# Performance work log

Measured on AMD Instinct MI355X. Metric: run time of the kernel, lower is better.

## Reference

```python
import jax, jax.numpy as jnp
import numpy as np

V, E, H, O, S, N = 32000, 256, 512, 32000, 128, 256

def setup_inputs() -> dict:
    key = jax.random.key(0)
    ks = jax.random.split(key, 12)
    s = 0.05
    return {
        'x': jax.random.randint(ks[0], (N, 1), 0, V),
        'encoder_outputs': jax.random.normal(ks[1], (N, S, 2 * H), jnp.float32),
        'hidden': jax.random.normal(ks[2], (1, N, H), jnp.float32),
        'cell': jax.random.normal(ks[3], (1, N, H), jnp.float32),
        'emb': jax.random.normal(ks[4], (V, E), jnp.float32) * s,
        'W_energy': jax.random.normal(ks[5], (1, 3 * H), jnp.float32) * s,
        'b_energy': jnp.zeros((1,), jnp.float32),
        'W_ih': jax.random.normal(ks[6], (4 * H, E + 2 * H), jnp.float32) * s,
        'W_hh': jax.random.normal(ks[7], (4 * H, H), jnp.float32) * s,
        'b_ih': jnp.zeros((4 * H,), jnp.float32),
        'b_hh': jnp.zeros((4 * H,), jnp.float32),
        'W_out': jax.random.normal(ks[8], (O, H), jnp.float32) * s,
        'b_out': jnp.zeros((O,), jnp.float32),
    }

def reference(x, encoder_outputs, hidden, cell, emb, W_energy, b_energy,
              W_ih, W_hh, b_ih, b_hh, W_out, b_out):
    # Dropout is identity at inference (eval mode).
    embedding = emb[x]                      # [N,1,E]
    n, s, _ = encoder_outputs.shape
    h = hidden[0]                            # [N,H] (num_layers==1)
    h_rep = jnp.broadcast_to(h[:, None, :], (n, s, h.shape[-1]))  # [N,S,H]
    feat = jnp.concatenate([h_rep, encoder_outputs], axis=-1)     # [N,S,3H]
    energy = jax.nn.relu(feat @ W_energy.T + b_energy)            # [N,S,1]
    attention = jax.nn.softmax(energy, axis=1)                    # softmax over seq
    context = jnp.einsum('nsk,nsl->nkl', attention, encoder_outputs)  # [N,1,2H]
    lstm_in = jnp.concatenate([context, embedding], axis=-1)[:, 0, :]  # [N,E+2H]
    gates = lstm_in @ W_ih.T + b_ih + h @ W_hh.T + b_hh           # [N,4H]
    i, f, g, o = jnp.split(gates, 4, axis=-1)                     # torch gate order
    i, f, o = jax.nn.sigmoid(i), jax.nn.sigmoid(f), jax.nn.sigmoid(o)
    g = jnp.tanh(g)
    c_new = f * cell[0] + i * g
    h_new = o * jnp.tanh(c_new)
    outputs = h_new[:, None, :]                                   # [N,1,H]
    predictions = outputs @ W_out.T + b_out                       # [N,1,O]
    return predictions, h_new[None], c_new[None]
```

## Files before the change

kernel.cpp:

```cpp
#include <hip/hip_runtime.h>
#include <hip/hip_bf16.h>

#define N_ 256
#define S_ 128
#define H_ 512
#define E_ 256
#define O_ 32000
#define KZ 1792
#define GJ 2048
#define KSPLIT 4
#define KCHUNK 448

typedef __attribute__((ext_vector_type(8))) short sv8;
typedef __attribute__((ext_vector_type(4))) float fv4;

__device__ __forceinline__ unsigned short f2bf(float f) {
  return __builtin_bit_cast(unsigned short, __float2bfloat16(f));
}

__device__ __forceinline__ sv8 pack8(fv4 a, fv4 b) {
  sv8 r;
  r[0] = (short)f2bf(a[0]); r[1] = (short)f2bf(a[1]);
  r[2] = (short)f2bf(a[2]); r[3] = (short)f2bf(a[3]);
  r[4] = (short)f2bf(b[0]); r[5] = (short)f2bf(b[1]);
  r[6] = (short)f2bf(b[2]); r[7] = (short)f2bf(b[3]);
  return r;
}

__global__ __launch_bounds__(1024) void k_attn(
    const int* __restrict__ x, const float* __restrict__ eo,
    const float* __restrict__ hid, const float* __restrict__ emb,
    const float* __restrict__ We, const float* __restrict__ be,
    const float* __restrict__ Wih, const float* __restrict__ Whh,
    unsigned short* __restrict__ Wgbf, unsigned short* __restrict__ z)
{
  if (blockIdx.y == 1) {
    const int tid = blockIdx.x * 1024 + threadIdx.x;
    for (int g = tid; g < 2048 * 224; g += 256 * 1024) {
      const int j = g / 224, c = g - j * 224;
      sv8* dst = (sv8*)(Wgbf + (size_t)j * KZ);
      if (c < 160) {
        const fv4* src = (const fv4*)(Wih + (size_t)j * 1280);
        dst[c] = pack8(src[2 * c], src[2 * c + 1]);
      } else {
        const int cc = c - 160;
        const fv4* src = (const fv4*)(Whh + (size_t)j * 512);
        dst[c] = pack8(src[2 * cc], src[2 * cc + 1]);
      }
    }
    return;
  }

  const int n = blockIdx.x;
  const int t = threadIdx.x;
  const int w = t >> 6;
  const int l = t & 63;

  __shared__ float s_red[16];
  __shared__ float s_l[16];
  __shared__ float s_ctx[16][1024];

  float hv = (t < 512) ? hid[(size_t)n * H_ + t] * We[t] : 0.f;
  #pragma unroll
  for (int off = 32; off >= 1; off >>= 1) hv += __shfl_xor(hv, off);
  if (l == 0) s_red[w] = hv;
  __syncthreads();
  float hWe = be[0];
  #pragma unroll
  for (int i = 0; i < 8; ++i) hWe += s_red[i];

  fv4 we0, we1, we2, we3;
  {
    const fv4* wp = (const fv4*)(We + H_);
    we0 = wp[l]; we1 = wp[l + 64]; we2 = wp[l + 128]; we3 = wp[l + 192];
  }

  float lsum = 0.f;
  fv4 c0 = {0,0,0,0}, c1 = {0,0,0,0}, c2 = {0,0,0,0}, c3 = {0,0,0,0};
  const float* eob = eo + ((size_t)n * S_ + w * 8) * 1024;
  #pragma unroll 2
  for (int i = 0; i < 8; ++i) {
    const fv4* p = (const fv4*)(eob + (size_t)i * 1024);
    fv4 v0 = p[l], v1 = p[l + 64], v2 = p[l + 128], v3 = p[l + 192];
    float d = 0.f;
    #pragma unroll
    for (int c = 0; c < 4; ++c)
      d += v0[c]*we0[c] + v1[c]*we1[c] + v2[c]*we2[c] + v3[c]*we3[c];
    #pragma unroll
    for (int off = 32; off >= 1; off >>= 1) d += __shfl_xor(d, off);
    const float pp = __expf(fmaxf(d + hWe, 0.f));
    lsum += pp;
    #pragma unroll
    for (int c = 0; c < 4; ++c) {
      c0[c] += pp*v0[c];
      c1[c] += pp*v1[c];
      c2[c] += pp*v2[c];
      c3[c] += pp*v3[c];
    }
  }
  if (l == 0) s_l[w] = lsum;
  {
    fv4* sc_ = (fv4*)s_ctx[w];
    sc_[l] = c0; sc_[l+64] = c1; sc_[l+128] = c2; sc_[l+192] = c3;
  }
  __syncthreads();

  float L = 0.f;
  #pragma unroll
  for (int i = 0; i < 16; ++i) L += s_l[i];
  const float rL = 1.f / L;

  float acc = 0.f;
  #pragma unroll
  for (int i = 0; i < 16; ++i) acc += s_ctx[i][t];
  unsigned short* zr = z + (size_t)n * KZ;
  zr[t] = f2bf(acc * rL);

  if (t < 256)       zr[1024 + t] = f2bf(emb[(size_t)x[n] * E_ + t]);
  else if (t < 768)  zr[1024 + t] = f2bf(hid[(size_t)n * H_ + (t - 256)]);
}

__global__ __launch_bounds__(256) void k_gates(
    const unsigned short* __restrict__ z, const unsigned short* __restrict__ Wgbf,
    float* __restrict__ part)
{
  const int j0 = blockIdx.x * 64;
  const int n0 = blockIdx.y * 64;
  const int kc = blockIdx.z * KCHUNK;
  const int t = threadIdx.x;
  const int w = t >> 6, l = t & 63;
  const int lr = l & 15, lg = l >> 4;
  const int jb = j0 + w * 16 + lr;

  const unsigned short* arow = z + kc + 8 * lg;
  const unsigned short* wrow = Wgbf + (size_t)jb * KZ + kc + 8 * lg;

  fv4 acc[4] = {{0,0,0,0},{0,0,0,0},{0,0,0,0},{0,0,0,0}};
  #pragma unroll
  for (int s = 0; s < 14; ++s) {
    const sv8 bf = *(const sv8*)(wrow + s * 32);
    #pragma unroll
    for (int f = 0; f < 4; ++f) {
      const sv8 af = *(const sv8*)(arow + (size_t)(n0 + f*16 + lr) * KZ + s * 32);
      acc[f] = __builtin_amdgcn_mfma_f32_16x16x32_bf16(af, bf, acc[f], 0, 0, 0);
    }
  }
  float* pp = part + (size_t)blockIdx.z * (N_ * GJ);
  #pragma unroll
  for (int f = 0; f < 4; ++f) {
    #pragma unroll
    for (int r = 0; r < 4; ++r)
      pp[(size_t)(n0 + f*16 + lg*4 + r) * GJ + jb] = acc[f][r];
  }
}

__global__ __launch_bounds__(256) void k_lstm(
    const float* __restrict__ part, const float* __restrict__ cell,
    const float* __restrict__ bih, const float* __restrict__ bhh,
    float* __restrict__ hout, float* __restrict__ cout,
    unsigned short* __restrict__ hbf)
{
  const int tid = blockIdx.x * 256 + threadIdx.x;
  const int n = tid >> 9, hh = tid & 511;
  const size_t base = (size_t)n * GJ;
  float ig = bih[hh]        + bhh[hh];
  float fg = bih[512 + hh]  + bhh[512 + hh];
  float gg = bih[1024 + hh] + bhh[1024 + hh];
  float og = bih[1536 + hh] + bhh[1536 + hh];
  #pragma unroll
  for (int k = 0; k < KSPLIT; ++k) {
    const float* p = part + (size_t)k * (N_ * GJ) + base;
    ig += p[hh];
    fg += p[512 + hh];
    gg += p[1024 + hh];
    og += p[1536 + hh];
  }
  ig = 1.f / (1.f + __expf(-ig));
  fg = 1.f / (1.f + __expf(-fg));
  og = 1.f / (1.f + __expf(-og));
  gg = tanhf(gg);
  const float c = fg * cell[tid] + ig * gg;
  const float h = og * tanhf(c);
  cout[tid] = c;
  hout[tid] = h;
  hbf[tid] = f2bf(h);
}

__global__ __launch_bounds__(512, 2) void k_pred(
    const unsigned short* __restrict__ hbf, const float* __restrict__ Wout,
    const float* __restrict__ bout, float* __restrict__ pred)
{
  __shared__ unsigned short Blds[64 * 512];
  const int o0 = blockIdx.x * 64;
  const int t = threadIdx.x;

  #pragma unroll
  for (int i = 0; i < 8; ++i) {
    const int g = t + i * 512;
    const int row = g >> 6, c = g & 63;
    const fv4* src = (const fv4*)(Wout + (size_t)(o0 + row) * H_ + c * 8);
    const sv8 v = pack8(src[0], src[1]);
    *(sv8*)((char*)Blds + row * 1024 + ((c * 16) ^ ((row & 7) << 4))) = v;
  }
  __syncthreads();

  const int w = t >> 6, l = t & 63;
  const int lr = l & 15, lg = l >> 4;
  const int nr = w * 32;

  fv4 acc[2][4] = {};
  #pragma unroll
  for (int kk = 0; kk < 16; ++kk) {
    sv8 a[2];
    #pragma unroll
    for (int f = 0; f < 2; ++f)
      a[f] = *(const sv8*)(hbf + (size_t)(nr + f*16 + lr) * H_ + kk*32 + 8*lg);
    #pragma unroll
    for (int fo = 0; fo < 4; ++fo) {
      const int row = fo * 16 + lr;
      const sv8 b = *(const sv8*)((const char*)Blds + row * 1024 +
                                  ((kk*64 + lg*16) ^ ((row & 7) << 4)));
      #pragma unroll
      for (int f = 0; f < 2; ++f)
        acc[f][fo] = __builtin_amdgcn_mfma_f32_16x16x32_bf16(a[f], b, acc[f][fo], 0, 0, 0);
    }
  }
  #pragma unroll
  for (int fo = 0; fo < 4; ++fo) {
    const int oo = o0 + fo*16 + lr;
    const float bo = bout[oo];
    #pragma unroll
    for (int f = 0; f < 2; ++f) {
      #pragma unroll
      for (int r = 0; r < 4; ++r)
        pred[(size_t)(nr + f*16 + lg*4 + r) * O_ + oo] = acc[f][fo][r] + bo;
    }
  }
}

extern "C" void kernel_launch(void* const* d_in, const int* in_sizes, int n_in,
                              void* d_out, int out_size, void* d_ws, size_t ws_size,
                              hipStream_t stream) {
  const int*   x    = (const int*)  d_in[0];
  const float* eo   = (const float*)d_in[1];
  const float* hid  = (const float*)d_in[2];
  const float* cell = (const float*)d_in[3];
  const float* emb  = (const float*)d_in[4];
  const float* We   = (const float*)d_in[5];
  const float* be   = (const float*)d_in[6];
  const float* Wih  = (const float*)d_in[7];
  const float* Whh  = (const float*)d_in[8];
  const float* bih  = (const float*)d_in[9];
  const float* bhh  = (const float*)d_in[10];
  const float* Wout = (const float*)d_in[11];
  const float* bout = (const float*)d_in[12];

  float* pred = (float*)d_out;
  float* hout = pred + (size_t)N_ * O_;
  float* cout = hout + (size_t)N_ * H_;

  unsigned short* z    = (unsigned short*)d_ws;
  unsigned short* hbf  = z + (size_t)N_ * KZ;
  float* part = (float*)(hbf + (size_t)N_ * H_);
  unsigned short* Wgbf = (unsigned short*)(part + (size_t)KSPLIT * N_ * GJ);

  k_attn <<<dim3(256, 2), 1024, 0, stream>>>(x, eo, hid, emb, We, be,
                                             Wih, Whh, Wgbf, z);
  k_gates<<<dim3(32, 4, KSPLIT), 256, 0, stream>>>(z, Wgbf, part);
  k_lstm <<<512, 256, 0, stream>>>(part, cell, bih, bhh, hout, cout, hbf);
  k_pred <<<500, 512, 0, stream>>>(hbf, Wout, bout, pred);
}
```

Before: 89.35 us.

## Fuse attention, gates, LSTM and projection into one cooperative persistent kernel

```diff
diff --git a/kernel.cpp b/kernel.cpp
--- a/kernel.cpp
+++ b/kernel.cpp
@@ -1,5 +1,8 @@
 #include <hip/hip_runtime.h>
 #include <hip/hip_bf16.h>
+#include <hip/hip_cooperative_groups.h>
+
+namespace cg = cooperative_groups;
 
 #define N_ 256
 #define S_ 128
@@ -8,8 +11,8 @@
 #define O_ 32000
 #define KZ 1792
 #define GJ 2048
-#define KSPLIT 4
-#define KCHUNK 448
+#define KSPLIT 8
+#define KCHUNK 224
 
 typedef __attribute__((ext_vector_type(8))) short sv8;
 typedef __attribute__((ext_vector_type(4))) float fv4;
@@ -27,16 +30,126 @@
   return r;
 }
 
-__global__ __launch_bounds__(1024) void k_attn(
+__device__ __forceinline__ void pred_stage(const float* __restrict__ Wout, int o0,
+                                           unsigned char* buf, int t) {
+  #pragma unroll
+  for (int i = 0; i < 4; ++i) {
+    const int g = t + i * 1024;
+    const int row = g >> 6, c = g & 63;
+    const fv4* src = (const fv4*)(Wout + (size_t)(o0 + row) * H_ + c * 8);
+    const sv8 v = pack8(src[0], src[1]);
+    *(sv8*)(buf + row * 1024 + ((c * 16) ^ ((row & 7) << 4))) = v;
+  }
+}
+
+__device__ __forceinline__ void pred_compute(const unsigned short* __restrict__ hbf,
+    const float* __restrict__ bout, float* __restrict__ pred, int o0,
+    const unsigned char* buf, int w, int lr, int lg) {
+  const int nr = w * 16;
+  fv4 acc[4] = {};
+  #pragma unroll
+  for (int kk = 0; kk < 16; ++kk) {
+    const sv8 a = *(const sv8*)(hbf + (size_t)(nr + lr) * H_ + kk * 32 + 8 * lg);
+    #pragma unroll
+    for (int fo = 0; fo < 4; ++fo) {
+      const int row = fo * 16 + lr;
+      const sv8 bb = *(const sv8*)(buf + row * 1024 +
+                                   ((kk * 64 + lg * 16) ^ ((row & 7) << 4)));
+      acc[fo] = __builtin_amdgcn_mfma_f32_16x16x32_bf16(a, bb, acc[fo], 0, 0, 0);
+    }
+  }
+  #pragma unroll
+  for (int fo = 0; fo < 4; ++fo) {
+    const int oo = o0 + fo * 16 + lr;
+    const float bo = bout[oo];
+    #pragma unroll
+    for (int r = 0; r < 4; ++r)
+      pred[(size_t)(nr + lg * 4 + r) * O_ + oo] = acc[fo][r] + bo;
+  }
+}
+
+__global__ __launch_bounds__(1024) void k_mega(
     const int* __restrict__ x, const float* __restrict__ eo,
-    const float* __restrict__ hid, const float* __restrict__ emb,
-    const float* __restrict__ We, const float* __restrict__ be,
-    const float* __restrict__ Wih, const float* __restrict__ Whh,
-    unsigned short* __restrict__ Wgbf, unsigned short* __restrict__ z)
+    const float* __restrict__ hid, const float* __restrict__ cell,
+    const float* __restrict__ emb, const float* __restrict__ We,
+    const float* __restrict__ be, const float* __restrict__ Wih,
+    const float* __restrict__ Whh, const float* __restrict__ bih,
+    const float* __restrict__ bhh, const float* __restrict__ Wout,
+    const float* __restrict__ bout,
+    unsigned short* __restrict__ z, unsigned short* __restrict__ hbf,
+    float* __restrict__ part, unsigned short* __restrict__ Wgbf,
+    float* __restrict__ pred, float* __restrict__ hout, float* __restrict__ cout)
 {
-  if (blockIdx.y == 1) {
-    const int tid = blockIdx.x * 1024 + threadIdx.x;
-    for (int g = tid; g < 2048 * 224; g += 256 * 1024) {
+  cg::grid_group grid = cg::this_grid();
+  const int b = blockIdx.x;
+  const int t = threadIdx.x;
+  const int w = t >> 6, l = t & 63;
+  const int lr = l & 15, lg = l >> 4;
+
+  __shared__ __align__(16) unsigned char smem[131072];
+  __shared__ float s_red[16], s_l[16];
+
+  {
+    const int n = b;
+    float* s_ctx = (float*)smem;
+
+    float hv = (t < 512) ? hid[(size_t)n * H_ + t] * We[t] : 0.f;
+    #pragma unroll
+    for (int off = 32; off >= 1; off >>= 1) hv += __shfl_xor(hv, off);
+    if (l == 0) s_red[w] = hv;
+    __syncthreads();
+    float hWe = be[0];
+    #pragma unroll
+    for (int i = 0; i < 8; ++i) hWe += s_red[i];
+
+    fv4 we0, we1, we2, we3;
+    {
+      const fv4* wp = (const fv4*)(We + H_);
+      we0 = wp[l]; we1 = wp[l + 64]; we2 = wp[l + 128]; we3 = wp[l + 192];
+    }
+
+    float lsum = 0.f;
+    fv4 c0 = {0,0,0,0}, c1 = {0,0,0,0}, c2 = {0,0,0,0}, c3 = {0,0,0,0};
+    const float* eob = eo + ((size_t)n * S_ + w * 8) * 1024;
+    #pragma unroll 2
+    for (int i = 0; i < 8; ++i) {
+      const fv4* p = (const fv4*)(eob + (size_t)i * 1024);
+      fv4 v0 = p[l], v1 = p[l + 64], v2 = p[l + 128], v3 = p[l + 192];
+      float d = 0.f;
+      #pragma unroll
+      for (int c = 0; c < 4; ++c)
+        d += v0[c]*we0[c] + v1[c]*we1[c] + v2[c]*we2[c] + v3[c]*we3[c];
+      #pragma unroll
+      for (int off = 32; off >= 1; off >>= 1) d += __shfl_xor(d, off);
+      const float pp = __expf(fmaxf(d + hWe, 0.f));
+      lsum += pp;
+      #pragma unroll
+      for (int c = 0; c < 4; ++c) {
+        c0[c] += pp*v0[c]; c1[c] += pp*v1[c];
+        c2[c] += pp*v2[c]; c3[c] += pp*v3[c];
+      }
+    }
+    if (l == 0) s_l[w] = lsum;
+    {
+      fv4* sc_ = (fv4*)(s_ctx + w * 1024);
+      sc_[l] = c0; sc_[l+64] = c1; sc_[l+128] = c2; sc_[l+192] = c3;
+    }
+    __syncthreads();
+
+    float L = 0.f;
+    #pragma unroll
+    for (int i = 0; i < 16; ++i) L += s_l[i];
+    const float rL = 1.f / L;
+
+    float acc = 0.f;
+    #pragma unroll
+    for (int i = 0; i < 16; ++i) acc += s_ctx[i * 1024 + t];
+    unsigned short* zr = z + (size_t)n * KZ;
+    zr[t] = f2bf(acc * rL);
+    if (t < 256)       zr[1024 + t] = f2bf(emb[(size_t)x[n] * E_ + t]);
+    else if (t < 768)  zr[1024 + t] = f2bf(hid[(size_t)n * H_ + (t - 256)]);
+
+    for (int g = b * 1024 + t; g < 2048 * 224; g += 256 * 1024) {
       const int j = g / 224, c = g - j * 224;
       sv8* dst = (sv8*)(Wgbf + (size_t)j * KZ);
       if (c < 160) {
@@ -48,192 +161,82 @@
         dst[c] = pack8(src[2 * cc], src[2 * cc + 1]);
       }
     }
-    return;
-  }
-
-  const int n = blockIdx.x;
-  const int t = threadIdx.x;
-  const int w = t >> 6;
-  const int l = t & 63;
-
-  __shared__ float s_red[16];
-  __shared__ float s_l[16];
-  __shared__ float s_ctx[16][1024];
-
-  float hv = (t < 512) ? hid[(size_t)n * H_ + t] * We[t] : 0.f;
-  #pragma unroll
-  for (int off = 32; off >= 1; off >>= 1) hv += __shfl_xor(hv, off);
-  if (l == 0) s_red[w] = hv;
-  __syncthreads();
-  float hWe = be[0];
-  #pragma unroll
-  for (int i = 0; i < 8; ++i) hWe += s_red[i];
-
-  fv4 we0, we1, we2, we3;
-  {
-    const fv4* wp = (const fv4*)(We + H_);
-    we0 = wp[l]; we1 = wp[l + 64]; we2 = wp[l + 128]; we3 = wp[l + 192];
-  }
-
-  float lsum = 0.f;
-  fv4 c0 = {0,0,0,0}, c1 = {0,0,0,0}, c2 = {0,0,0,0}, c3 = {0,0,0,0};
-  const float* eob = eo + ((size_t)n * S_ + w * 8) * 1024;
-  #pragma unroll 2
-  for (int i = 0; i < 8; ++i) {
-    const fv4* p = (const fv4*)(eob + (size_t)i * 1024);
-    fv4 v0 = p[l], v1 = p[l + 64], v2 = p[l + 128], v3 = p[l + 192];
-    float d = 0.f;
-    #pragma unroll
-    for (int c = 0; c < 4; ++c)
-      d += v0[c]*we0[c] + v1[c]*we1[c] + v2[c]*we2[c] + v3[c]*we3[c];
-    #pragma unroll
-    for (int off = 32; off >= 1; off >>= 1) d += __shfl_xor(d, off);
-    const float pp = __expf(fmaxf(d + hWe, 0.f));
-    lsum += pp;
-    #pragma unroll
-    for (int c = 0; c < 4; ++c) {
-      c0[c] += pp*v0[c];
-      c1[c] += pp*v1[c];
-      c2[c] += pp*v2[c];
-      c3[c] += pp*v3[c];
-    }
-  }
-  if (l == 0) s_l[w] = lsum;
-  {
-    fv4* sc_ = (fv4*)s_ctx[w];
-    sc_[l] = c0; sc_[l+64] = c1; sc_[l+128] = c2; sc_[l+192] = c3;
-  }
-  __syncthreads();
-
-  float L = 0.f;
-  #pragma unroll
-  for (int i = 0; i < 16; ++i) L += s_l[i];
-  const float rL = 1.f / L;
-
-  float acc = 0.f;
-  #pragma unroll
-  for (int i = 0; i < 16; ++i) acc += s_ctx[i][t];
-  unsigned short* zr = z + (size_t)n * KZ;
-  zr[t] = f2bf(acc * rL);
-
-  if (t < 256)       zr[1024 + t] = f2bf(emb[(size_t)x[n] * E_ + t]);
-  else if (t < 768)  zr[1024 + t] = f2bf(hid[(size_t)n * H_ + (t - 256)]);
-}
-
-__global__ __launch_bounds__(256) void k_gates(
-    const unsigned short* __restrict__ z, const unsigned short* __restrict__ Wgbf,
-    float* __restrict__ part)
-{
-  const int j0 = blockIdx.x * 64;
-  const int n0 = blockIdx.y * 64;
-  const int kc = blockIdx.z * KCHUNK;
-  const int t = threadIdx.x;
-  const int w = t >> 6, l = t & 63;
-  const int lr = l & 15, lg = l >> 4;
-  const int jb = j0 + w * 16 + lr;
-
-  const unsigned short* arow = z + kc + 8 * lg;
-  const unsigned short* wrow = Wgbf + (size_t)jb * KZ + kc + 8 * lg;
-
-  fv4 acc[4] = {{0,0,0,0},{0,0,0,0},{0,0,0,0},{0,0,0,0}};
-  #pragma unroll
-  for (int s = 0; s < 14; ++s) {
-    const sv8 bf = *(const sv8*)(wrow + s * 32);
+  }
+  grid.sync();
+
+  {
+    const int quad = w >> 2, wq = w & 3;
+    const int tile = b * 4 + quad;
+    const int j0   = (tile & 31) * 64;
+    const int rest = tile >> 5;
+    const int n0   = (rest & 3) * 64;
+    const int kidx = rest >> 2;
+    const int kc   = kidx * KCHUNK;
+    const int jb   = j0 + wq * 16 + lr;
+
+    const unsigned short* arow = z + kc + 8 * lg;
+    const unsigned short* wrow = Wgbf + (size_t)jb * KZ + kc + 8 * lg;
+
+    fv4 acc[4] = {{0,0,0,0},{0,0,0,0},{0,0,0,0},{0,0,0,0}};
+    #pragma unroll
+    for (int s = 0; s < 7; ++s) {
+      const sv8 bf = *(const sv8*)(wrow + s * 32);
+      #pragma unroll
+      for (int f = 0; f < 4; ++f) {
+        const sv8 af = *(const sv8*)(arow + (size_t)(n0 + f*16 + lr) * KZ + s * 32);
+        acc[f] = __builtin_amdgcn_mfma_f32_16x16x32_bf16(af, bf, acc[f], 0, 0, 0);
+      }
+    }
+    float* pp = part + (size_t)kidx * (N_ * GJ);
     #pragma unroll
     for (int f = 0; f < 4; ++f) {
-      const sv8 af = *(const sv8*)(arow + (size_t)(n0 + f*16 + lr) * KZ + s * 32);
-      acc[f] = __builtin_amdgcn_mfma_f32_16x16x32_bf16(af, bf, acc[f], 0, 0, 0);
-    }
-  }
-  float* pp = part + (size_t)blockIdx.z * (N_ * GJ);
-  #pragma unroll
-  for (int f = 0; f < 4; ++f) {
-    #pragma unroll
-    for (int r = 0; r < 4; ++r)
-      pp[(size_t)(n0 + f*16 + lg*4 + r) * GJ + jb] = acc[f][r];
-  }
-}
-
-__global__ __launch_bounds__(256) void k_lstm(
-    const float* __restrict__ part, const float* __restrict__ cell,
-    const float* __restrict__ bih, const float* __restrict__ bhh,
-    float* __restrict__ hout, float* __restrict__ cout,
-    unsigned short* __restrict__ hbf)
-{
-  const int tid = blockIdx.x * 256 + threadIdx.x;
-  const int n = tid >> 9, hh = tid & 511;
-  const size_t base = (size_t)n * GJ;
-  float ig = bih[hh]        + bhh[hh];
-  float fg = bih[512 + hh]  + bhh[512 + hh];
-  float gg = bih[1024 + hh] + bhh[1024 + hh];
-  float og = bih[1536 + hh] + bhh[1536 + hh];
-  #pragma unroll
-  for (int k = 0; k < KSPLIT; ++k) {
-    const float* p = part + (size_t)k * (N_ * GJ) + base;
-    ig += p[hh];
-    fg += p[512 + hh];
-    gg += p[1024 + hh];
-    og += p[1536 + hh];
-  }
-  ig = 1.f / (1.f + __expf(-ig));
-  fg = 1.f / (1.f + __expf(-fg));
-  og = 1.f / (1.f + __expf(-og));
-  gg = tanhf(gg);
-  const float c = fg * cell[tid] + ig * gg;
-  const float h = og * tanhf(c);
-  cout[tid] = c;
-  hout[tid] = h;
-  hbf[tid] = f2bf(h);
-}
-
-__global__ __launch_bounds__(512, 2) void k_pred(
-    const unsigned short* __restrict__ hbf, const float* __restrict__ Wout,
-    const float* __restrict__ bout, float* __restrict__ pred)
-{
-  __shared__ unsigned short Blds[64 * 512];
-  const int o0 = blockIdx.x * 64;
-  const int t = threadIdx.x;
-
-  #pragma unroll
-  for (int i = 0; i < 8; ++i) {
-    const int g = t + i * 512;
-    const int row = g >> 6, c = g & 63;
-    const fv4* src = (const fv4*)(Wout + (size_t)(o0 + row) * H_ + c * 8);
-    const sv8 v = pack8(src[0], src[1]);
-    *(sv8*)((char*)Blds + row * 1024 + ((c * 16) ^ ((row & 7) << 4))) = v;
-  }
-  __syncthreads();
-
-  const int w = t >> 6, l = t & 63;
-  const int lr = l & 15, lg = l >> 4;
-  const int nr = w * 32;
-
-  fv4 acc[2][4] = {};
-  #pragma unroll
-  for (int kk = 0; kk < 16; ++kk) {
-    sv8 a[2];
-    #pragma unroll
-    for (int f = 0; f < 2; ++f)
-      a[f] = *(const sv8*)(hbf + (size_t)(nr + f*16 + lr) * H_ + kk*32 + 8*lg);
-    #pragma unroll
-    for (int fo = 0; fo < 4; ++fo) {
-      const int row = fo * 16 + lr;
-      const sv8 b = *(const sv8*)((const char*)Blds + row * 1024 +
-                                  ((kk*64 + lg*16) ^ ((row & 7) << 4)));
-      #pragma unroll
-      for (int f = 0; f < 2; ++f)
-        acc[f][fo] = __builtin_amdgcn_mfma_f32_16x16x32_bf16(a[f], b, acc[f][fo], 0, 0, 0);
-    }
-  }
-  #pragma unroll
-  for (int fo = 0; fo < 4; ++fo) {
-    const int oo = o0 + fo*16 + lr;
-    const float bo = bout[oo];
-    #pragma unroll
-    for (int f = 0; f < 2; ++f) {
       #pragma unroll
       for (int r = 0; r < 4; ++r)
-        pred[(size_t)(nr + f*16 + lg*4 + r) * O_ + oo] = acc[f][fo][r] + bo;
+        pp[(size_t)(n0 + f*16 + lg*4 + r) * GJ + jb] = acc[f][r];
+    }
+  }
+  grid.sync();
+
+  {
+    const int tid = b * 1024 + t;
+    if (tid < N_ * H_) {
+      const int n = tid >> 9, hh = tid & 511;
+      const size_t base = (size_t)n * GJ;
+      float ig = bih[hh]        + bhh[hh];
+      float fg = bih[512 + hh]  + bhh[512 + hh];
+      float gg = bih[1024 + hh] + bhh[1024 + hh];
+      float og = bih[1536 + hh] + bhh[1536 + hh];
+      #pragma unroll
+      for (int k = 0; k < KSPLIT; ++k) {
+        const float* p = part + (size_t)k * (N_ * GJ) + base;
+        ig += p[hh];
+        fg += p[512 + hh];
+        gg += p[1024 + hh];
+        og += p[1536 + hh];
+      }
+      ig = 1.f / (1.f + __expf(-ig));
+      fg = 1.f / (1.f + __expf(-fg));
+      og = 1.f / (1.f + __expf(-og));
+      gg = tanhf(gg);
+      const float c = fg * cell[tid] + ig * gg;
+      const float h = og * tanhf(c);
+      cout[tid] = c;
+      hout[tid] = h;
+      hbf[tid] = f2bf(h);
+    }
+  }
+  grid.sync();
+
+  {
+    const int o0a = b * 64;
+    const int o1  = b + 256;
+    pred_stage(Wout, o0a, smem, t);
+    __syncthreads();
+    if (o1 < 500) pred_stage(Wout, o1 * 64, smem + 65536, t);
+    pred_compute(hbf, bout, pred, o0a, smem, w, lr, lg);
+    if (o1 < 500) {
+      __syncthreads();
+      pred_compute(hbf, bout, pred, o1 * 64, smem + 65536, w, lr, lg);
     }
   }
 }
@@ -264,9 +267,13 @@
   float* part = (float*)(hbf + (size_t)N_ * H_);
   unsigned short* Wgbf = (unsigned short*)(part + (size_t)KSPLIT * N_ * GJ);
 
-  k_attn <<<dim3(256, 2), 1024, 0, stream>>>(x, eo, hid, emb, We, be,
-                                             Wih, Whh, Wgbf, z);
-  k_gates<<<dim3(32, 4, KSPLIT), 256, 0, stream>>>(z, Wgbf, part);
-  k_lstm <<<512, 256, 0, stream>>>(part, cell, bih, bhh, hout, cout, hbf);
-  k_pred <<<500, 512, 0, stream>>>(hbf, Wout, bout, pred);
-}
+  void* args[] = {
+    (void*)&x, (void*)&eo, (void*)&hid, (void*)&cell, (void*)&emb,
+    (void*)&We, (void*)&be, (void*)&Wih, (void*)&Whh, (void*)&bih,
+    (void*)&bhh, (void*)&Wout, (void*)&bout,
+    (void*)&z, (void*)&hbf, (void*)&part, (void*)&Wgbf,
+    (void*)&pred, (void*)&hout, (void*)&cout
+  };
+  hipLaunchCooperativeKernel((const void*)k_mega, dim3(256), dim3(1024),
+                             args, 0, stream);
+}
```

New measurement: 188.4 us. +110.8%, slower.
